# Kernel optimization log

Hardware: AMD Instinct MI355X
Metric: run time of the kernel (lower is better)

Reference implementation:

```python
import jax, jax.numpy as jnp
import numpy as np

EPS = 1e-5
TAU = 2.0

# Heaviside spike with spikingjelly's default Sigmoid surrogate gradient (alpha=4)
@jax.custom_vjp
def spike(x):
    return (x >= 0.0).astype(x.dtype)

def _spike_fwd(x):
    return (x >= 0.0).astype(x.dtype), x

def _spike_bwd(x, g):
    a = 4.0
    s = jax.nn.sigmoid(a * x)
    return (g * a * s * (1.0 - s),)

spike.defvjp(_spike_fwd, _spike_bwd)

def lif(x_seq, v_th, v_reset):
    """Multi-step LIF (decay_input=True, detach_reset=True). v_reset=None -> soft reset."""
    def step(v, x):
        if v_reset is None:
            v = v + (x - v) / TAU
        else:
            v = v + (x - (v - v_reset)) / TAU
        s = spike(v - v_th)
        sd = jax.lax.stop_gradient(s)  # detach_reset=True
        if v_reset is None:
            v = v - sd * v_th
        else:
            v = (1.0 - sd) * v + sd * v_reset
        return v, s
    _, s_seq = jax.lax.scan(step, jnp.zeros_like(x_seq[0]), x_seq)
    return s_seq

def conv2d(x, w, groups=1):
    return jax.lax.conv_general_dilated(x, w, (1, 1), 'VALID',
        dimension_numbers=('NCHW', 'OIHW', 'NCHW'), feature_group_count=groups)

def bn(x, p):
    # p: [4, C] = (weight, bias, running_mean, running_var); inference-mode BN
    w, b, m, v = p
    inv = w * jax.lax.rsqrt(v + EPS)
    return x * inv[None, :, None, None] + (b - m * inv)[None, :, None, None]

def bn_pad(x, p):
    # BNAndPadLayer(pad_pixels=1): BN then pad 1px border with the BN of zeros
    y = bn(x, p)
    w, b, m, v = p
    pv = (b - m * w * jax.lax.rsqrt(v + EPS))[None, :, None, None]
    y = jnp.pad(y, ((0, 0), (0, 0), (1, 1), (1, 1)))
    y = y.at[:, :, :1, :].set(pv)
    y = y.at[:, :, -1:, :].set(pv)
    y = y.at[:, :, :, :1].set(pv)
    y = y.at[:, :, :, -1:].set(pv)
    return y

def repconv(x, w1, bn1, dw, pw, bn2):
    y = conv2d(x, w1)                       # 1x1 in->in
    y = bn_pad(y, bn1)                      # BN + 1px pad
    y = conv2d(y, dw, groups=dw.shape[0])   # depthwise 3x3, valid
    y = conv2d(y, pw)                       # 1x1 in->out
    return bn(y, bn2)

def setup_inputs() -> dict:
    T, B, C, H, W = 4, 16, 384, 32, 32
    key = jax.random.key(0)
    ks = iter(jax.random.split(key, 32))
    def bn_params(c):
        k1, k2, k3, k4 = jax.random.split(next(ks), 4)
        return jnp.stack([
            1.0 + 0.1 * jax.random.normal(k1, (c,)),
            0.1 * jax.random.normal(k2, (c,)),
            0.1 * jax.random.normal(k3, (c,)),
            jax.random.uniform(k4, (c,), minval=0.5, maxval=1.5)]).astype(jnp.float32)
    def conv_w(shape, fan_in):
        return (jax.random.normal(next(ks), shape) / np.sqrt(fan_in)).astype(jnp.float32)
    return dict(
        x=jax.random.normal(next(ks), (T, B, C, H, W), dtype=jnp.float32),
        r1_w1=conv_w((C, C, 1, 1), C),
        r1_bn1=bn_params(C),
        r1_dw=conv_w((C, 1, 3, 3), 9),
        r1_pw=conv_w((2 * C, C, 1, 1), C),
        r1_bn2=bn_params(2 * C),
        qkv_bn=bn_params(2 * C),
        r2_w1=conv_w((C, C, 1, 1), C),
        r2_bn1=bn_params(C),
        r2_dw=conv_w((C, 1, 3, 3), 9),
        r2_pw=conv_w((C, C, 1, 1), C),
        r2_bn2=bn_params(C),
        proj_bn=bn_params(C),
        scale=jnp.array([0.1], dtype=jnp.float32),
    )

def reference(x, r1_w1, r1_bn1, r1_dw, r1_pw, r1_bn2, qkv_bn,
              r2_w1, r2_bn1, r2_dw, r2_pw, r2_bn2, proj_bn, scale):
    T, B, C, H, W = x.shape
    xs = lif(x, 1.0, 0.0)                                  # shortcut_lif (hard reset)
    y = repconv(xs.reshape(T * B, C, H, W), r1_w1, r1_bn1, r1_dw, r1_pw, r1_bn2)
    y = bn(y, qkv_bn).reshape(T, B, 2 * C, H, W)           # qkv_conv outer BN
    qk, v = y[:, :, :C], y[:, :, C:]
    qk = lif(qk, 1.0, None)                                # qk_lif (soft reset)
    qk = qk.sum(axis=(-1, -2), keepdims=True)              # jit_sum over H,W -> [T,B,C,1,1]
    qk = lif(qk, 0.5, 0.0)                                 # talking_heads_lif (th=0.5, hard)
    v = lif(v, 1.0, None)                                  # v_lif (soft reset)
    out = qk * v                                           # jit_mul broadcast over H,W
    out = repconv(out.reshape(T * B, C, H, W), r2_w1, r2_bn1, r2_dw, r2_pw, r2_bn2)
    out = bn(out, proj_bn).reshape(T, B, C, H, W)          # proj_conv outer BN
    out = lif(out, 1.0, None)                              # proj_lif (soft reset)
    return out * scale
```

## Files before the change

kernel.cpp:

```cpp
#include <hip/hip_runtime.h>

typedef _Float16 f16;
typedef __attribute__((ext_vector_type(8))) _Float16 f16x8;
typedef __attribute__((ext_vector_type(4))) float f32x4;

#define TT 4
#define BB 16
#define CC 384

__device__ __forceinline__ float lif_soft(float x, float& v) {
  v = __fadd_rn(v, __fmul_rn(__fsub_rn(x, v), 0.5f));
  float s = (__fsub_rn(v, 1.0f) >= 0.0f) ? 1.0f : 0.0f;
  v = __fsub_rn(v, s);
  return s;
}
__device__ __forceinline__ float lif_hard(float x, float& v, float vth) {
  v = __fadd_rn(v, __fmul_rn(__fsub_rn(x, v), 0.5f));
  float s = (__fsub_rn(v, vth) >= 0.0f) ? 1.0f : 0.0f;
  if (s != 0.0f) v = 0.0f;
  return s;
}

__global__ __launch_bounds__(768) void k_prep(const float* __restrict__ bn1,
                                              const float* __restrict__ bn2,
                                              const float* __restrict__ qkv,
                                              const float* __restrict__ rbn1,
                                              const float* __restrict__ rbn2,
                                              const float* __restrict__ proj,
                                              float* __restrict__ par) {
  int c = threadIdx.x;
  float* s1 = par;          float* o1 = par + 384;
  float* sA = par + 768;    float* oA = par + 1536;
  float* s2 = par + 2304;   float* o2 = par + 2688;
  float* sB = par + 3072;   float* oB = par + 3456;
  if (c < 384) {
    double a = (double)bn1[c] / sqrt((double)bn1[3*384+c] + 1e-5);
    s1[c] = (float)a;
    o1[c] = (float)((double)bn1[384+c] - (double)bn1[2*384+c]*a);
    double a2 = (double)rbn1[c] / sqrt((double)rbn1[3*384+c] + 1e-5);
    s2[c] = (float)a2;
    o2[c] = (float)((double)rbn1[384+c] - (double)rbn1[2*384+c]*a2);
    double a3 = (double)rbn2[c] / sqrt((double)rbn2[3*384+c] + 1e-5);
    double b3 = (double)rbn2[384+c] - (double)rbn2[2*384+c]*a3;
    double a4 = (double)proj[c] / sqrt((double)proj[3*384+c] + 1e-5);
    double b4 = (double)proj[384+c] - (double)proj[2*384+c]*a4;
    sB[c] = (float)(a3*a4);
    oB[c] = (float)(b3*a4 + b4);
  }
  if (c < 768) {
    double a5 = (double)bn2[c] / sqrt((double)bn2[3*768+c] + 1e-5);
    double b5 = (double)bn2[768+c] - (double)bn2[2*768+c]*a5;
    double a6 = (double)qkv[c] / sqrt((double)qkv[3*768+c] + 1e-5);
    double b6 = (double)qkv[768+c] - (double)qkv[2*768+c]*a6;
    sA[c] = (float)(a5*a6);
    oA[c] = (float)(b5*a6 + b6);
  }
}

__global__ __launch_bounds__(256) void k_wsplit(const float* __restrict__ w,
                                                f16* __restrict__ wa, f16* __restrict__ wb, int n) {
  int i = blockIdx.x * 256 + threadIdx.x;
  if (i < n) {
    float x = w[i];
    f16 a = (f16)x;
    wa[i] = a;
    wb[i] = (f16)((x - (float)a) * 2048.0f);
  }
}

__global__ __launch_bounds__(256) void k_lif_in(const float* __restrict__ x, f16* __restrict__ xs) {
  __shared__ float tile[64][65];
  const int p0 = blockIdx.x * 64, c0 = blockIdx.y * 64, b = blockIdx.z;
  const int l = threadIdx.x & 63, q = threadIdx.x >> 6;
  float v[16];
  #pragma unroll
  for (int j = 0; j < 16; ++j) v[j] = 0.0f;
  for (int t = 0; t < TT; ++t) {
    __syncthreads();
    #pragma unroll
    for (int j = 0; j < 16; ++j) {
      int ci = q + j*4;
      tile[ci][l] = x[(((size_t)(t*BB + b)*CC + c0 + ci) << 10) + p0 + l];
    }
    __syncthreads();
    #pragma unroll
    for (int j = 0; j < 16; ++j) {
      int pi = q + j*4;
      float s = lif_hard(tile[l][pi], v[j], 1.0f);
      xs[((size_t)(t*BB + b)*1024 + p0 + pi)*CC + c0 + l] = (f16)s;
    }
  }
}

__device__ __forceinline__ void stage_arr(const f16* __restrict__ g, int row0, int k0,
                                          f16* dst, int lane, int i0, int i1) {
  #pragma unroll
  for (int i = i0; i < i1; ++i) {
    int loff = i*1024 + lane*16;
    int row = loff >> 6, col = loff & 63;
    int scol = col ^ (((row >> 1) & 3) << 4);
    const char* src = (const char*)g + (size_t)(row0 + row)*768 + (size_t)(k0*2) + scol;
    __builtin_amdgcn_global_load_lds((const __attribute__((address_space(1))) void*)src,
                                     (__attribute__((address_space(3))) void*)((char*)dst + i*1024),
                                     16, 0, 0);
  }
}

__device__ __forceinline__ f16x8 fragld32(const f16* arr, int row, int fq) {
  int off = row*64 + ((fq*16) ^ (((row >> 1) & 3) << 4));
  return *(const f16x8*)((const char*)arr + off);
}

template<int NP>
__global__ __launch_bounds__(256, 2) void k_gemm(const f16* __restrict__ X1, const f16* __restrict__ X2,
    const f16* __restrict__ Wa, const f16* __restrict__ Wb,
    const float* __restrict__ scale, const float* __restrict__ bias,
    float* __restrict__ out0, float* __restrict__ out1) {
  constexpr int ARR = (NP == 3) ? 4 : 3;
  __shared__ __align__(16) f16 lds[2*ARR*4096];
  const int gx = gridDim.x;
  const int bid = blockIdx.y * gx + blockIdx.x;
  const int chunk = (gx * gridDim.y) >> 3;
  const int nb = (bid & 7) * chunk + (bid >> 3);
  const int m0 = (nb / gx) * 128;
  const int o0 = (nb % gx) * 128;
  const int lane = threadIdx.x & 63, wid = threadIdx.x >> 6;
  const int wr = wid >> 1, wc = wid & 1;
  const int fr = lane & 15, fq = lane >> 4;
  f32x4 acc_h[4][4], acc_l[4][4];
  #pragma unroll
  for (int i = 0; i < 4; ++i)
    #pragma unroll
    for (int j = 0; j < 4; ++j) { acc_h[i][j] = (f32x4){0,0,0,0}; acc_l[i][j] = (f32x4){0,0,0,0}; }

  auto stage_all = [&](int buf, int k0) {
    f16* base = lds + buf*(ARR*4096);
    if (NP == 3) {
      if (wid == 0)      stage_arr(X1, m0, k0, base,          lane, 0, 8);
      else if (wid == 1) stage_arr(X2, m0, k0, base + 4096,   lane, 0, 8);
      else if (wid == 2) stage_arr(Wa, o0, k0, base + 2*4096, lane, 0, 8);
      else               stage_arr(Wb, o0, k0, base + 3*4096, lane, 0, 8);
    } else {
      if (wid == 0)      stage_arr(X1, m0, k0, base,          lane, 0, 4);
      else if (wid == 1) stage_arr(X1, m0, k0, base,          lane, 4, 8);
      else if (wid == 2) stage_arr(Wa, o0, k0, base + 4096,   lane, 0, 8);
      else               stage_arr(Wb, o0, k0, base + 2*4096, lane, 0, 8);
    }
  };

  stage_all(0, 0);
  __syncthreads();

  for (int it = 0; it < 12; ++it) {
    const int cur = it & 1;
    if (it < 11) stage_all(cur ^ 1, (it + 1)*32);
    const f16* bX1 = lds + cur*(ARR*4096);
    const f16* bW1 = (NP == 3) ? bX1 + 2*4096 : bX1 + 4096;
    const f16* bW2 = (NP == 3) ? bX1 + 3*4096 : bX1 + 2*4096;
    f16x8 a1[4], b1[4], b2[4];
    #pragma unroll
    for (int mi = 0; mi < 4; ++mi) a1[mi] = fragld32(bX1, wr*64 + mi*16 + fr, fq);
    #pragma unroll
    for (int oi = 0; oi < 4; ++oi) {
      b1[oi] = fragld32(bW1, wc*64 + oi*16 + fr, fq);
      b2[oi] = fragld32(bW2, wc*64 + oi*16 + fr, fq);
    }
    if (NP == 3) {
      const f16* bX2 = bX1 + 4096;
      f16x8 a2[4];
      #pragma unroll
      for (int mi = 0; mi < 4; ++mi) a2[mi] = fragld32(bX2, wr*64 + mi*16 + fr, fq);
      #pragma unroll
      for (int mi = 0; mi < 4; ++mi)
        #pragma unroll
        for (int oi = 0; oi < 4; ++oi) {
          acc_h[mi][oi] = __builtin_amdgcn_mfma_f32_16x16x32_f16(a1[mi], b1[oi], acc_h[mi][oi], 0, 0, 0);
          acc_l[mi][oi] = __builtin_amdgcn_mfma_f32_16x16x32_f16(a1[mi], b2[oi], acc_l[mi][oi], 0, 0, 0);
          acc_l[mi][oi] = __builtin_amdgcn_mfma_f32_16x16x32_f16(a2[mi], b1[oi], acc_l[mi][oi], 0, 0, 0);
        }
    } else {
      #pragma unroll
      for (int mi = 0; mi < 4; ++mi)
        #pragma unroll
        for (int oi = 0; oi < 4; ++oi) {
          acc_h[mi][oi] = __builtin_amdgcn_mfma_f32_16x16x32_f16(a1[mi], b1[oi], acc_h[mi][oi], 0, 0, 0);
          acc_l[mi][oi] = __builtin_amdgcn_mfma_f32_16x16x32_f16(a1[mi], b2[oi], acc_l[mi][oi], 0, 0, 0);
        }
    }
    __syncthreads();
  }

  #pragma unroll
  for (int oi = 0; oi < 4; ++oi) {
    int o = o0 + wc*64 + oi*16 + fr;
    float sc = scale[o], bi = bias[o];
    float* op = out0; int oc = o;
    if (o >= 384) { op = out1; oc = o - 384; }
    #pragma unroll
    for (int mi = 0; mi < 4; ++mi) {
      f32x4 h = acc_h[mi][oi], lo2 = acc_l[mi][oi];
      #pragma unroll
      for (int r = 0; r < 4; ++r) {
        int m = m0 + wr*64 + mi*16 + fq*4 + r;
        float y = fmaf(0.00048828125f, lo2[r], h[r]);
        op[(size_t)m*384 + oc] = fmaf(y, sc, bi);
      }
    }
  }
}

__global__ __launch_bounds__(256) void k_dw(const float* __restrict__ in, const float* __restrict__ wd,
                                            const float* __restrict__ pv,
                                            f16* __restrict__ outA, f16* __restrict__ outB) {
  const int ct = blockIdx.x, h = blockIdx.y, n = blockIdx.z;
  const int c = ct*64 + (threadIdx.x & 63);
  const int wq = threadIdx.x >> 6;
  float w9[9];
  #pragma unroll
  for (int i = 0; i < 9; ++i) w9[i] = wd[c*9 + i];
  const float pvc = pv[c];
  const float* base = in + (size_t)n*1024*CC;
  for (int wi = 0; wi < 8; ++wi) {
    int w = wq*8 + wi;
    float acc = 0.0f;
    #pragma unroll
    for (int dh = -1; dh <= 1; ++dh)
      #pragma unroll
      for (int dw = -1; dw <= 1; ++dw) {
        int hh = h + dh, ww = w + dw;
        float vv = ((unsigned)hh < 32u && (unsigned)ww < 32u) ? base[(size_t)(hh*32 + ww)*CC + c] : pvc;
        acc = fmaf(w9[(dh+1)*3 + dw + 1], vv, acc);
      }
    f16 a = (f16)acc;
    size_t off = ((size_t)n*1024 + h*32 + w)*CC + c;
    outA[off] = a;
    outB[off] = (f16)((acc - (float)a) * 2048.0f);
  }
}

__global__ __launch_bounds__(256) void k_qksum(const float* __restrict__ y6qk, float* __restrict__ partial) {
  __shared__ float red[4][4][64];
  const int ps = blockIdx.x, ct = blockIdx.y, b = blockIdx.z;
  const int l = threadIdx.x & 63, pg = threadIdx.x >> 6;
  const int c = ct*64 + l;
  float sums[4] = {0,0,0,0};
  for (int i = 0; i < 32; ++i) {
    int p = ps*128 + pg*32 + i;
    float v = 0.0f;
    #pragma unroll
    for (int t = 0; t < TT; ++t) {
      float xv = y6qk[((size_t)(t*BB + b)*1024 + p)*CC + c];
      sums[t] += lif_soft(xv, v);
    }
  }
  #pragma unroll
  for (int t = 0; t < TT; ++t) red[pg][t][l] = sums[t];
  __syncthreads();
  int t2 = threadIdx.x >> 6;
  float tot = red[0][t2][l] + red[1][t2][l] + red[2][t2][l] + red[3][t2][l];
  partial[(((size_t)ps*4 + t2)*BB + b)*CC + c] = tot;
}

__global__ __launch_bounds__(256) void k_gate(const float* __restrict__ partial, float* __restrict__ gate) {
  int g = blockIdx.x*256 + threadIdx.x;
  int b = g / CC, c = g % CC;
  float sums[4];
  #pragma unroll
  for (int t = 0; t < TT; ++t) {
    float s = 0.0f;
    for (int ps = 0; ps < 8; ++ps) s += partial[(((size_t)ps*4 + t)*BB + b)*CC + c];
    sums[t] = s;
  }
  float v = 0.0f;
  #pragma unroll
  for (int t = 0; t < TT; ++t)
    gate[(size_t)(t*BB + b)*CC + c] = lif_hard(sums[t], v, 0.5f);
}

__global__ __launch_bounds__(256) void k_vatt(const float* __restrict__ y6v, const float* __restrict__ gate,
                                              f16* __restrict__ att) {
  const int psl = blockIdx.x, ct = blockIdx.y, b = blockIdx.z;
  const int l = threadIdx.x & 63, pg = threadIdx.x >> 6;
  const int c = ct*64 + l;
  float g4[4];
  #pragma unroll
  for (int t = 0; t < TT; ++t) g4[t] = gate[(size_t)(t*BB + b)*CC + c];
  for (int i = 0; i < 16; ++i) {
    int p = psl*64 + pg*16 + i;
    float v = 0.0f;
    #pragma unroll
    for (int t = 0; t < TT; ++t) {
      size_t off = ((size_t)(t*BB + b)*1024 + p)*CC + c;
      float s = lif_soft(y6v[off], v);
      att[off] = (f16)(s * g4[t]);
    }
  }
}

__global__ __launch_bounds__(256) void k_lif_out(const float* __restrict__ z, const float* __restrict__ scalep,
                                                 float* __restrict__ out) {
  __shared__ float tile[64][65];
  const int p0 = blockIdx.x * 64, c0 = blockIdx.y * 64, b = blockIdx.z;
  const int l = threadIdx.x & 63, q = threadIdx.x >> 6;
  const float sc = scalep[0];
  float v[16];
  #pragma unroll
  for (int j = 0; j < 16; ++j) v[j] = 0.0f;
  for (int t = 0; t < TT; ++t) {
    __syncthreads();
    #pragma unroll
    for (int j = 0; j < 16; ++j) {
      int pi = q + j*4;
      tile[pi][l] = z[((size_t)(t*BB + b)*1024 + p0 + pi)*CC + c0 + l];
    }
    __syncthreads();
    #pragma unroll
    for (int j = 0; j < 16; ++j) {
      int ci = q + j*4;
      float s = lif_soft(tile[l][ci], v[j]) * sc;
      out[(((size_t)(t*BB + b))*CC + c0 + ci)*1024 + p0 + l] = s;
    }
  }
}

extern "C" void kernel_launch(void* const* d_in, const int* in_sizes, int n_in,
                              void* d_out, int out_size, void* d_ws, size_t ws_size,
                              hipStream_t stream) {
  const float* x      = (const float*)d_in[0];
  const float* r1_w1  = (const float*)d_in[1];
  const float* r1_bn1 = (const float*)d_in[2];
  const float* r1_dw  = (const float*)d_in[3];
  const float* r1_pw  = (const float*)d_in[4];
  const float* r1_bn2 = (const float*)d_in[5];
  const float* qkv_bn = (const float*)d_in[6];
  const float* r2_w1  = (const float*)d_in[7];
  const float* r2_bn1 = (const float*)d_in[8];
  const float* r2_dw  = (const float*)d_in[9];
  const float* r2_pw  = (const float*)d_in[10];
  const float* r2_bn2 = (const float*)d_in[11];
  const float* proj_bn= (const float*)d_in[12];
  const float* scale  = (const float*)d_in[13];

  float* ws = (float*)d_ws;
  const size_t SEG = 12582912;
  float* W0f = ws;
  float* W1  = ws + SEG;
  float* W2f = ws + 3*SEG;
  float* W3  = ws + 4*SEG;
  f16* xs   = (f16*)W0f;
  f16* p1a  = (f16*)W0f;
  f16* p2b  = (f16*)W0f;
  f16* p1b  = (f16*)W2f;
  f16* att  = (f16*)W2f;
  f16* p2a  = (f16*)W2f;
  float* t1   = W1;
  float* y6qk = W1;
  float* t2   = W1;
  float* y6v  = W3;
  float* z    = W3;

  f16* wsp = (f16*)(ws + 6*SEG);
  f16* w1a = wsp,            *w1b = wsp + 147456;
  f16* pwa = wsp + 294912,   *pwb = wsp + 589824;
  float* partial = (float*)wsp;
  float* gate    = (float*)wsp + 196608;
  f16* q1a = wsp,            *q1b = wsp + 147456;
  f16* qpa = wsp + 294912,   *qpb = wsp + 442368;

  float* par = ws + 6*SEG + 442368;
  float* s1 = par,        *o1 = par + 384;
  float* sA = par + 768,  *oA = par + 1536;
  float* s2 = par + 2304, *o2 = par + 2688;
  float* sB = par + 3072, *oB = par + 3456;

  k_prep<<<1, 768, 0, stream>>>(r1_bn1, r1_bn2, qkv_bn, r2_bn1, r2_bn2, proj_bn, par);
  k_wsplit<<<576, 256, 0, stream>>>(r1_w1, w1a, w1b, 147456);
  k_wsplit<<<1152, 256, 0, stream>>>(r1_pw, pwa, pwb, 294912);
  k_lif_in<<<dim3(16, 6, 16), 256, 0, stream>>>(x, xs);
  k_gemm<2><<<dim3(3, 512), 256, 0, stream>>>(xs, (const f16*)nullptr, w1a, w1b, s1, o1, t1, t1);
  k_dw<<<dim3(6, 32, 64), 256, 0, stream>>>(t1, r1_dw, o1, p1a, p1b);
  k_gemm<3><<<dim3(6, 512), 256, 0, stream>>>(p1a, p1b, pwa, pwb, sA, oA, y6qk, y6v);
  k_qksum<<<dim3(8, 6, 16), 256, 0, stream>>>(y6qk, partial);
  k_gate<<<24, 256, 0, stream>>>(partial, gate);
  k_vatt<<<dim3(16, 6, 16), 256, 0, stream>>>(y6v, gate, att);
  k_wsplit<<<576, 256, 0, stream>>>(r2_w1, q1a, q1b, 147456);
  k_wsplit<<<576, 256, 0, stream>>>(r2_pw, qpa, qpb, 147456);
  k_gemm<2><<<dim3(3, 512), 256, 0, stream>>>(att, (const f16*)nullptr, q1a, q1b, s2, o2, t2, t2);
  k_dw<<<dim3(6, 32, 64), 256, 0, stream>>>(t2, r2_dw, o2, p2a, p2b);
  k_gemm<3><<<dim3(3, 512), 256, 0, stream>>>(p2a, p2b, qpa, qpb, sB, oB, z, z);
  k_lif_out<<<dim3(16, 6, 16), 256, 0, stream>>>(z, scale, (float*)d_out);
}
```

Measured before the change: 572.2 us.

## Use partial vmcnt waits to overlap next-tile LDS staging with MFMA compute

Replaces the full __syncthreads before compute with an explicit s_waitcnt vmcnt(N) that waits only for the current buffer's global->LDS loads, leaving the next buffer's loads in flight, then a raw s_barrier. It also rebalances staging in the NP!=3 path so every wave issues 6 loads instead of an uneven 4/4/8/8 split. The aim is to let prefetch overlap compute instead of draining all outstanding memory at each barrier. It relies on hand-counted vmcnt values matching the compiler's instruction order, which could break correctness if other vector memory ops get interleaved.

```diff
diff --git a/kernel.cpp b/kernel.cpp
--- a/kernel.cpp
+++ b/kernel.cpp
@@ -92,18 +92,15 @@
   }
 }
 
-__device__ __forceinline__ void stage_arr(const f16* __restrict__ g, int row0, int k0,
-                                          f16* dst, int lane, int i0, int i1) {
-  #pragma unroll
-  for (int i = i0; i < i1; ++i) {
-    int loff = i*1024 + lane*16;
-    int row = loff >> 6, col = loff & 63;
-    int scol = col ^ (((row >> 1) & 3) << 4);
-    const char* src = (const char*)g + (size_t)(row0 + row)*768 + (size_t)(k0*2) + scol;
-    __builtin_amdgcn_global_load_lds((const __attribute__((address_space(1))) void*)src,
-                                     (__attribute__((address_space(3))) void*)((char*)dst + i*1024),
-                                     16, 0, 0);
-  }
+__device__ __forceinline__ void stage_one(const f16* __restrict__ g, int row0, int k0,
+                                          f16* dst, int lane, int i) {
+  int loff = i*1024 + lane*16;
+  int row = loff >> 6, col = loff & 63;
+  int scol = col ^ (((row >> 1) & 3) << 4);
+  const char* src = (const char*)g + (size_t)(row0 + row)*768 + (size_t)(k0*2) + scol;
+  __builtin_amdgcn_global_load_lds((const __attribute__((address_space(1))) void*)src,
+                                   (__attribute__((address_space(3))) void*)((char*)dst + i*1024),
+                                   16, 0, 0);
 }
 
 __device__ __forceinline__ f16x8 fragld32(const f16* arr, int row, int fq) {
@@ -136,24 +133,36 @@
   auto stage_all = [&](int buf, int k0) {
     f16* base = lds + buf*(ARR*4096);
     if (NP == 3) {
-      if (wid == 0)      stage_arr(X1, m0, k0, base,          lane, 0, 8);
-      else if (wid == 1) stage_arr(X2, m0, k0, base + 4096,   lane, 0, 8);
-      else if (wid == 2) stage_arr(Wa, o0, k0, base + 2*4096, lane, 0, 8);
-      else               stage_arr(Wb, o0, k0, base + 3*4096, lane, 0, 8);
+      const f16* g = (wid == 0) ? X1 : (wid == 1) ? X2 : (wid == 2) ? Wa : Wb;
+      int row0 = (wid <= 1) ? m0 : o0;
+      f16* dst = base + wid*4096;
+      #pragma unroll
+      for (int i = 0; i < 8; ++i) stage_one(g, row0, k0, dst, lane, i);
     } else {
-      if (wid == 0)      stage_arr(X1, m0, k0, base,          lane, 0, 4);
-      else if (wid == 1) stage_arr(X1, m0, k0, base,          lane, 4, 8);
-      else if (wid == 2) stage_arr(Wa, o0, k0, base + 4096,   lane, 0, 8);
-      else               stage_arr(Wb, o0, k0, base + 2*4096, lane, 0, 8);
+      #pragma unroll
+      for (int j = 0; j < 6; ++j) {
+        int s = wid*6 + j;
+        int arr = s >> 3, inst = s & 7;
+        const f16* g = (arr == 0) ? X1 : (arr == 1) ? Wa : Wb;
+        int row0 = (arr == 0) ? m0 : o0;
+        stage_one(g, row0, k0, base + arr*4096, lane, inst);
+      }
     }
   };
 
   stage_all(0, 0);
-  __syncthreads();
 
   for (int it = 0; it < 12; ++it) {
     const int cur = it & 1;
     if (it < 11) stage_all(cur ^ 1, (it + 1)*32);
+    if (it < 11) {
+      if constexpr (NP == 3) asm volatile("s_waitcnt vmcnt(8)" ::: "memory");
+      else                   asm volatile("s_waitcnt vmcnt(6)" ::: "memory");
+    } else {
+      asm volatile("s_waitcnt vmcnt(0)" ::: "memory");
+    }
+    __builtin_amdgcn_sched_barrier(0);
+    __builtin_amdgcn_s_barrier();
     const f16* bX1 = lds + cur*(ARR*4096);
     const f16* bW1 = (NP == 3) ? bX1 + 2*4096 : bX1 + 4096;
     const f16* bW2 = (NP == 3) ? bX1 + 3*4096 : bX1 + 2*4096;
@@ -187,7 +196,7 @@
           acc_l[mi][oi] = __builtin_amdgcn_mfma_f32_16x16x32_f16(a1[mi], b2[oi], acc_l[mi][oi], 0, 0, 0);
         }
     }
-    __syncthreads();
+    __builtin_amdgcn_s_barrier();
   }
 
   #pragma unroll
```

After: 725.3 us. 26.7% more time.

## Fuse qk/v LIF and qk-sum into GEMM epilogue, apply gate in next GEMM

Applied to the files above, without the earlier changes.

The second GEMM now gathers rows so that each 128-row tile holds all 4 timesteps of 32 pixels. This lets its epilogue run the soft-reset LIF in registers/LDS and emit either fp16 v spikes or fp16 per-slice qk spike partial sums. The talking-heads gate is folded into the following GEMM by scaling A fragments per K chunk, so k_qksum and k_vatt are removed. The goal is to drop the large fp32 y6 round trip through global memory. In exchange the GEMM epilogue gets heavier, and partial sums are stored in fp16 and gathered over 64 slices.

```diff
diff --git a/kernel.cpp b/kernel.cpp
--- a/kernel.cpp
+++ b/kernel.cpp
@@ -92,14 +92,18 @@
   }
 }
 
-__device__ __forceinline__ void stage_arr(const f16* __restrict__ g, int row0, int k0,
-                                          f16* dst, int lane, int i0, int i1) {
+template<int EPI>
+__device__ __forceinline__ void stage_arrT(const f16* __restrict__ g, int m0, int b_, int p0,
+                                           int k0, f16* dst, int lane, int i0, int i1, bool isX) {
   #pragma unroll
   for (int i = i0; i < i1; ++i) {
     int loff = i*1024 + lane*16;
     int row = loff >> 6, col = loff & 63;
     int scol = col ^ (((row >> 1) & 3) << 4);
-    const char* src = (const char*)g + (size_t)(row0 + row)*768 + (size_t)(k0*2) + scol;
+    int gm;
+    if (EPI == 1 && isX) gm = ((row >> 5) << 14) + (b_ << 10) + p0 + (row & 31);
+    else                 gm = m0 + row;
+    const char* src = (const char*)g + (size_t)gm*768 + (size_t)(k0*2) + scol;
     __builtin_amdgcn_global_load_lds((const __attribute__((address_space(1))) void*)src,
                                      (__attribute__((address_space(3))) void*)((char*)dst + i*1024),
                                      16, 0, 0);
@@ -111,19 +115,22 @@
   return *(const f16x8*)((const char*)arr + off);
 }
 
-template<int NP>
+template<int NP, int EPI, int GATE>
 __global__ __launch_bounds__(256, 2) void k_gemm(const f16* __restrict__ X1, const f16* __restrict__ X2,
     const f16* __restrict__ Wa, const f16* __restrict__ Wb,
     const float* __restrict__ scale, const float* __restrict__ bias,
-    float* __restrict__ out0, float* __restrict__ out1) {
+    float* __restrict__ out0, float* __restrict__ out1,
+    const f16* __restrict__ gatep, f16* __restrict__ sOut, f16* __restrict__ part) {
   constexpr int ARR = (NP == 3) ? 4 : 3;
   __shared__ __align__(16) f16 lds[2*ARR*4096];
   const int gx = gridDim.x;
   const int bid = blockIdx.y * gx + blockIdx.x;
   const int chunk = (gx * gridDim.y) >> 3;
   const int nb = (bid & 7) * chunk + (bid >> 3);
-  const int m0 = (nb / gx) * 128;
   const int o0 = (nb % gx) * 128;
+  const int mb = nb / gx;
+  const int m0 = mb * 128;
+  const int b_ = mb >> 5, p0 = (mb & 31) << 5;
   const int lane = threadIdx.x & 63, wid = threadIdx.x >> 6;
   const int wr = wid >> 1, wc = wid & 1;
   const int fr = lane & 15, fq = lane >> 4;
@@ -136,17 +143,24 @@
   auto stage_all = [&](int buf, int k0) {
     f16* base = lds + buf*(ARR*4096);
     if (NP == 3) {
-      if (wid == 0)      stage_arr(X1, m0, k0, base,          lane, 0, 8);
-      else if (wid == 1) stage_arr(X2, m0, k0, base + 4096,   lane, 0, 8);
-      else if (wid == 2) stage_arr(Wa, o0, k0, base + 2*4096, lane, 0, 8);
-      else               stage_arr(Wb, o0, k0, base + 3*4096, lane, 0, 8);
+      if (wid == 0)      stage_arrT<EPI>(X1, m0, b_, p0, k0, base,          lane, 0, 8, true);
+      else if (wid == 1) stage_arrT<EPI>(X2, m0, b_, p0, k0, base + 4096,   lane, 0, 8, true);
+      else if (wid == 2) stage_arrT<EPI>(Wa, o0, b_, p0, k0, base + 2*4096, lane, 0, 8, false);
+      else               stage_arrT<EPI>(Wb, o0, b_, p0, k0, base + 3*4096, lane, 0, 8, false);
     } else {
-      if (wid == 0)      stage_arr(X1, m0, k0, base,          lane, 0, 4);
-      else if (wid == 1) stage_arr(X1, m0, k0, base,          lane, 4, 8);
-      else if (wid == 2) stage_arr(Wa, o0, k0, base + 4096,   lane, 0, 8);
-      else               stage_arr(Wb, o0, k0, base + 2*4096, lane, 0, 8);
+      if (wid == 0)      stage_arrT<EPI>(X1, m0, b_, p0, k0, base,          lane, 0, 4, true);
+      else if (wid == 1) stage_arrT<EPI>(X1, m0, b_, p0, k0, base,          lane, 4, 8, true);
+      else if (wid == 2) stage_arrT<EPI>(Wa, o0, b_, p0, k0, base + 4096,   lane, 0, 8, false);
+      else               stage_arrT<EPI>(Wb, o0, b_, p0, k0, base + 2*4096, lane, 0, 8, false);
     }
   };
+
+  const char* gbase = nullptr;
+  f16x8 g8{}, gn{};
+  if constexpr (GATE) {
+    gbase = (const char*)gatep + (size_t)(m0 >> 10)*768 + fq*16;
+    g8 = *(const f16x8*)gbase;
+  }
 
   stage_all(0, 0);
   __syncthreads();
@@ -154,12 +168,17 @@
   for (int it = 0; it < 12; ++it) {
     const int cur = it & 1;
     if (it < 11) stage_all(cur ^ 1, (it + 1)*32);
+    if constexpr (GATE) { if (it < 11) gn = *(const f16x8*)(gbase + (it + 1)*64); }
     const f16* bX1 = lds + cur*(ARR*4096);
     const f16* bW1 = (NP == 3) ? bX1 + 2*4096 : bX1 + 4096;
     const f16* bW2 = (NP == 3) ? bX1 + 3*4096 : bX1 + 2*4096;
     f16x8 a1[4], b1[4], b2[4];
     #pragma unroll
     for (int mi = 0; mi < 4; ++mi) a1[mi] = fragld32(bX1, wr*64 + mi*16 + fr, fq);
+    if constexpr (GATE) {
+      #pragma unroll
+      for (int mi = 0; mi < 4; ++mi) a1[mi] = a1[mi] * g8;
+    }
     #pragma unroll
     for (int oi = 0; oi < 4; ++oi) {
       b1[oi] = fragld32(bW1, wc*64 + oi*16 + fr, fq);
@@ -188,23 +207,71 @@
         }
     }
     __syncthreads();
-  }
-
-  #pragma unroll
-  for (int oi = 0; oi < 4; ++oi) {
-    int o = o0 + wc*64 + oi*16 + fr;
-    float sc = scale[o], bi = bias[o];
-    float* op = out0; int oc = o;
-    if (o >= 384) { op = out1; oc = o - 384; }
-    #pragma unroll
-    for (int mi = 0; mi < 4; ++mi) {
-      f32x4 h = acc_h[mi][oi], lo2 = acc_l[mi][oi];
-      #pragma unroll
-      for (int r = 0; r < 4; ++r) {
-        int m = m0 + wr*64 + mi*16 + fq*4 + r;
-        float y = fmaf(0.00048828125f, lo2[r], h[r]);
-        op[(size_t)m*384 + oc] = fmaf(y, sc, bi);
+    if constexpr (GATE) { if (it < 11) g8 = gn; }
+  }
+
+  if constexpr (EPI == 0) {
+    #pragma unroll
+    for (int oi = 0; oi < 4; ++oi) {
+      int o = o0 + wc*64 + oi*16 + fr;
+      float sc = scale[o], bi = bias[o];
+      float* op = out0; int oc = o;
+      if (o >= 384) { op = out1; oc = o - 384; }
+      #pragma unroll
+      for (int mi = 0; mi < 4; ++mi) {
+        f32x4 h = acc_h[mi][oi], lo2 = acc_l[mi][oi];
+        #pragma unroll
+        for (int r = 0; r < 4; ++r) {
+          int m = m0 + wr*64 + mi*16 + fq*4 + r;
+          float y = fmaf(0.00048828125f, lo2[r], h[r]);
+          op[(size_t)m*384 + oc] = fmaf(y, sc, bi);
+        }
       }
+    }
+  } else {
+    float* T = (float*)lds;
+    #pragma unroll
+    for (int oi = 0; oi < 4; ++oi) {
+      int ol = wc*64 + oi*16 + fr;
+      float sc = scale[o0 + ol], bi = bias[o0 + ol];
+      #pragma unroll
+      for (int mi = 0; mi < 4; ++mi) {
+        f32x4 h = acc_h[mi][oi], lo2 = acc_l[mi][oi];
+        #pragma unroll
+        for (int r = 0; r < 4; ++r) {
+          int R = wr*64 + mi*16 + fq*4 + r;
+          float y = fmaf(0.00048828125f, lo2[r], h[r]);
+          T[R*128 + ol] = fmaf(y, sc, bi);
+        }
+      }
+    }
+    __syncthreads();
+    const int tid = threadIdx.x;
+    const int oc = tid & 127, ph = tid >> 7;
+    if (o0 >= 384) {
+      const int ocg = (o0 - 384) + oc;
+      #pragma unroll
+      for (int i = 0; i < 16; ++i) {
+        int p = ph*16 + i;
+        float v = 0.0f;
+        #pragma unroll
+        for (int t = 0; t < TT; ++t) {
+          float s = lif_soft(T[(t*32 + p)*128 + oc], v);
+          sOut[((size_t)((t*16 + b_)*1024 + p0 + p))*384 + ocg] = (f16)s;
+        }
+      }
+    } else {
+      float ps4[4] = {0,0,0,0};
+      for (int i = 0; i < 16; ++i) {
+        int p = ph*16 + i;
+        float v = 0.0f;
+        #pragma unroll
+        for (int t = 0; t < TT; ++t) ps4[t] += lif_soft(T[(t*32 + p)*128 + oc], v);
+      }
+      int slice = (p0 >> 4) + ph;
+      #pragma unroll
+      for (int t = 0; t < TT; ++t)
+        part[(((size_t)slice*4 + t)*16 + b_)*384 + o0 + oc] = (f16)ps4[t];
     }
   }
 }
@@ -238,63 +305,20 @@
   }
 }
 
-__global__ __launch_bounds__(256) void k_qksum(const float* __restrict__ y6qk, float* __restrict__ partial) {
-  __shared__ float red[4][4][64];
-  const int ps = blockIdx.x, ct = blockIdx.y, b = blockIdx.z;
-  const int l = threadIdx.x & 63, pg = threadIdx.x >> 6;
-  const int c = ct*64 + l;
-  float sums[4] = {0,0,0,0};
-  for (int i = 0; i < 32; ++i) {
-    int p = ps*128 + pg*32 + i;
-    float v = 0.0f;
-    #pragma unroll
-    for (int t = 0; t < TT; ++t) {
-      float xv = y6qk[((size_t)(t*BB + b)*1024 + p)*CC + c];
-      sums[t] += lif_soft(xv, v);
-    }
-  }
-  #pragma unroll
-  for (int t = 0; t < TT; ++t) red[pg][t][l] = sums[t];
-  __syncthreads();
-  int t2 = threadIdx.x >> 6;
-  float tot = red[0][t2][l] + red[1][t2][l] + red[2][t2][l] + red[3][t2][l];
-  partial[(((size_t)ps*4 + t2)*BB + b)*CC + c] = tot;
-}
-
-__global__ __launch_bounds__(256) void k_gate(const float* __restrict__ partial, float* __restrict__ gate) {
+__global__ __launch_bounds__(256) void k_gate(const f16* __restrict__ partial, f16* __restrict__ gate16) {
   int g = blockIdx.x*256 + threadIdx.x;
   int b = g / CC, c = g % CC;
   float sums[4];
   #pragma unroll
   for (int t = 0; t < TT; ++t) {
     float s = 0.0f;
-    for (int ps = 0; ps < 8; ++ps) s += partial[(((size_t)ps*4 + t)*BB + b)*CC + c];
+    for (int ps = 0; ps < 64; ++ps) s += (float)partial[(((size_t)ps*4 + t)*BB + b)*CC + c];
     sums[t] = s;
   }
   float v = 0.0f;
   #pragma unroll
   for (int t = 0; t < TT; ++t)
-    gate[(size_t)(t*BB + b)*CC + c] = lif_hard(sums[t], v, 0.5f);
-}
-
-__global__ __launch_bounds__(256) void k_vatt(const float* __restrict__ y6v, const float* __restrict__ gate,
-                                              f16* __restrict__ att) {
-  const int psl = blockIdx.x, ct = blockIdx.y, b = blockIdx.z;
-  const int l = threadIdx.x & 63, pg = threadIdx.x >> 6;
-  const int c = ct*64 + l;
-  float g4[4];
-  #pragma unroll
-  for (int t = 0; t < TT; ++t) g4[t] = gate[(size_t)(t*BB + b)*CC + c];
-  for (int i = 0; i < 16; ++i) {
-    int p = psl*64 + pg*16 + i;
-    float v = 0.0f;
-    #pragma unroll
-    for (int t = 0; t < TT; ++t) {
-      size_t off = ((size_t)(t*BB + b)*1024 + p)*CC + c;
-      float s = lif_soft(y6v[off], v);
-      att[off] = (f16)(s * g4[t]);
-    }
-  }
+    gate16[((size_t)(t*BB + b))*CC + c] = (f16)lif_hard(sums[t], v, 0.5f);
 }
 
 __global__ __launch_bounds__(256) void k_lif_out(const float* __restrict__ z, const float* __restrict__ scalep,
@@ -347,46 +371,45 @@
   float* W1  = ws + SEG;
   float* W2f = ws + 3*SEG;
   float* W3  = ws + 4*SEG;
-  f16* xs   = (f16*)W0f;
-  f16* p1a  = (f16*)W0f;
-  f16* p2b  = (f16*)W0f;
-  f16* p1b  = (f16*)W2f;
-  f16* att  = (f16*)W2f;
-  f16* p2a  = (f16*)W2f;
-  float* t1   = W1;
-  float* y6qk = W1;
-  float* t2   = W1;
-  float* y6v  = W3;
-  float* z    = W3;
+  f16* xs  = (f16*)W0f;
+  f16* p1a = (f16*)W0f;
+  f16* p2b = (f16*)W0f;
+  f16* p1b = (f16*)W2f;
+  f16* p2a = (f16*)W2f;
+  float* t1  = W1;
+  f16*  s16  = (f16*)W1;
+  float* z   = W1;
+  float* t2  = W3;
 
   f16* wsp = (f16*)(ws + 6*SEG);
-  f16* w1a = wsp,            *w1b = wsp + 147456;
-  f16* pwa = wsp + 294912,   *pwb = wsp + 589824;
-  float* partial = (float*)wsp;
-  float* gate    = (float*)wsp + 196608;
-  f16* q1a = wsp,            *q1b = wsp + 147456;
-  f16* qpa = wsp + 294912,   *qpb = wsp + 442368;
-
-  float* par = ws + 6*SEG + 442368;
+  f16* w1a = wsp,              *w1b = wsp + 147456;
+  f16* pwa = wsp + 294912,     *pwb = wsp + 589824;
+  f16* q1a = wsp + 884736,     *q1b = wsp + 1032192;
+  f16* qpa = wsp + 1179648,    *qpb = wsp + 1327104;
+  f16* partial = wsp + 1474560;
+  f16* gate16  = wsp + 3047424;
+  float* par = (float*)(wsp + 3072000);
   float* s1 = par,        *o1 = par + 384;
   float* sA = par + 768,  *oA = par + 1536;
   float* s2 = par + 2304, *o2 = par + 2688;
   float* sB = par + 3072, *oB = par + 3456;
 
+  const f16* nf = (const f16*)nullptr;
+  f16* nf2 = (f16*)nullptr;
+
   k_prep<<<1, 768, 0, stream>>>(r1_bn1, r1_bn2, qkv_bn, r2_bn1, r2_bn2, proj_bn, par);
   k_wsplit<<<576, 256, 0, stream>>>(r1_w1, w1a, w1b, 147456);
   k_wsplit<<<1152, 256, 0, stream>>>(r1_pw, pwa, pwb, 294912);
-  k_lif_in<<<dim3(16, 6, 16), 256, 0, stream>>>(x, xs);
-  k_gemm<2><<<dim3(3, 512), 256, 0, stream>>>(xs, (const f16*)nullptr, w1a, w1b, s1, o1, t1, t1);
-  k_dw<<<dim3(6, 32, 64), 256, 0, stream>>>(t1, r1_dw, o1, p1a, p1b);
-  k_gemm<3><<<dim3(6, 512), 256, 0, stream>>>(p1a, p1b, pwa, pwb, sA, oA, y6qk, y6v);
-  k_qksum<<<dim3(8, 6, 16), 256, 0, stream>>>(y6qk, partial);
-  k_gate<<<24, 256, 0, stream>>>(partial, gate);
-  k_vatt<<<dim3(16, 6, 16), 256, 0, stream>>>(y6v, gate, att);
   k_wsplit<<<576, 256, 0, stream>>>(r2_w1, q1a, q1b, 147456);
   k_wsplit<<<576, 256, 0, stream>>>(r2_pw, qpa, qpb, 147456);
-  k_gemm<2><<<dim3(3, 512), 256, 0, stream>>>(att, (const f16*)nullptr, q1a, q1b, s2, o2, t2, t2);
+  k_lif_in<<<dim3(16, 6, 16), 256, 0, stream>>>(x, xs);
+  k_gemm<2,0,0><<<dim3(3, 512), 256, 0, stream>>>(xs, nf, w1a, w1b, s1, o1, t1, t1, nf, nf2, nf2);
+  k_dw<<<dim3(6, 32, 64), 256, 0, stream>>>(t1, r1_dw, o1, p1a, p1b);
+  k_gemm<3,1,0><<<dim3(6, 512), 256, 0, stream>>>(p1a, p1b, pwa, pwb, sA, oA,
+                                                  (float*)nullptr, (float*)nullptr, nf, s16, partial);
+  k_gate<<<24, 256, 0, stream>>>(partial, gate16);
+  k_gemm<2,0,1><<<dim3(3, 512), 256, 0, stream>>>(s16, nf, q1a, q1b, s2, o2, t2, t2, gate16, nf2, nf2);
   k_dw<<<dim3(6, 32, 64), 256, 0, stream>>>(t2, r2_dw, o2, p2a, p2b);
-  k_gemm<3><<<dim3(3, 512), 256, 0, stream>>>(p2a, p2b, qpa, qpb, sB, oB, z, z);
+  k_gemm<3,0,0><<<dim3(3, 512), 256, 0, stream>>>(p2a, p2b, qpa, qpb, sB, oB, z, z, nf, nf2, nf2);
   k_lif_out<<<dim3(16, 6, 16), 256, 0, stream>>>(z, scale, (float*)d_out);
 }
```

Result: faster. 544.3 us (-4.9%).
